# Optimization experiments

Measured on AMD Instinct MI355X. Metric: run time of the kernel, lower is better.

## Reference

```python
import jax, jax.numpy as jnp
import numpy as np

N, M, D = 1024, 1024, 512


def setup_inputs() -> dict:
    key = jax.random.key(0)
    ks = jax.random.split(key, 12)
    s = 1.0 / np.sqrt(D)
    return {
        "q": jax.random.normal(ks[0], (N, D), jnp.float32),
        "k": jax.random.normal(ks[1], (M, D), jnp.float32),
        "v": jax.random.normal(ks[2], (M, D), jnp.float32),
        "mask": jax.random.randint(ks[3], (N, M), 0, 2) > 0,
        "Wq": jax.random.normal(ks[4], (D, D), jnp.float32) * s,
        "bq": jax.random.normal(ks[5], (D,), jnp.float32) * s,
        "Wk": jax.random.normal(ks[6], (D, D), jnp.float32) * s,
        "bk": jax.random.normal(ks[7], (D,), jnp.float32) * s,
        "Wv": jax.random.normal(ks[8], (D, D), jnp.float32) * s,
        "bv": jax.random.normal(ks[9], (D,), jnp.float32) * s,
        "Ww": jax.random.normal(ks[10], (D,), jnp.float32) * s,
        "bw": jax.random.normal(ks[11], (1,), jnp.float32) * s,
    }


def reference(q, k, v, mask, Wq, bq, Wk, bk, Wv, bv, Ww, bw):
    # Linear projections (torch Linear: x @ W.T + b)
    qp = q @ Wq.T + bq  # [N, D]
    kp = k @ Wk.T + bk  # [M, D]
    vp = v @ Wv.T + bv  # [M, D]
    # Bahdanau additive score: W(tanh(q_n + k_m)) -> [N, M]
    h = jnp.tanh(qp[:, None, :] + kp[None, :, :])  # [N, M, D]
    scores = jnp.einsum('nmd,d->nm', h, Ww) + bw[0]
    scores = jnp.where(mask, scores, jnp.float32(-1000000.0))
    attn = jax.nn.softmax(scores, axis=1)  # softmax over M (dim 1)
    context = jnp.einsum('nm,md->nd', attn, vp)  # [N, D]
    return context
```

## Files before the change

kernel.cpp:

```cpp
#include <hip/hip_runtime.h>
#include <hip/hip_bf16.h>
#include <float.h>


#define NROWS 1024
#define DDIM  512
#define MDIM  1024

typedef __attribute__((ext_vector_type(8))) short s8v;
typedef __attribute__((ext_vector_type(4))) float f4v;
typedef __attribute__((ext_vector_type(2))) float v2f;

__device__ __forceinline__ ushort f2bf(float f) {
    unsigned u = __float_as_uint(f);
    u = u + 0x7FFFu + ((u >> 16) & 1u);
    return (ushort)(u >> 16);
}
__device__ __forceinline__ float bf2f(ushort h) {
    return __uint_as_float(((unsigned)h) << 16);
}

__device__ __forceinline__ void load_lds16(const float* g, float* l) {
    __builtin_amdgcn_global_load_lds(
        (const __attribute__((address_space(1))) void*)g,
        (__attribute__((address_space(3))) void*)l, 16, 0, 0);
}

__global__ __launch_bounds__(256) void proj_gemm(
    const float* __restrict__ q, const float* __restrict__ kk_,
    const float* __restrict__ v,
    const float* __restrict__ Wq, const float* __restrict__ bq,
    const float* __restrict__ Wk, const float* __restrict__ bk,
    const float* __restrict__ Wv, const float* __restrict__ bv,
    float* __restrict__ eq, float* __restrict__ ekT,
    ushort* __restrict__ vph, ushort* __restrict__ vpl,
    float* __restrict__ S, float CS)
{
    __shared__ ushort Ah[4096], Al[4096], Bh[4096], Bl[4096];

    const float* A; const float* B; const float* bias;
    int biasRow;
    if (blockIdx.z == 0)      { A = q;   B = Wq;  bias = bq; biasRow = 0; }
    else if (blockIdx.z == 1) { A = Wk;  B = kk_; bias = bk; biasRow = 1; }
    else                      { A = Wv;  B = v;   bias = bv; biasRow = 1; }

    const int bi = (blockIdx.z == 0) ? blockIdx.x : blockIdx.y;
    const int bj = (blockIdx.z == 0) ? blockIdx.y : blockIdx.x;

    const int t    = threadIdx.x;
    const int lane = t & 63;
    const int w    = t >> 6;
    const int lm   = lane & 15;
    const int lq   = lane >> 4;
    const int i0   = bi * 64;
    const int j0   = bj * 64;
    const int mh   = (w >> 1) * 32;
    const int nh   = (w & 1) * 32;

    if (blockIdx.z == 0) {
        const int jb = blockIdx.x * 8 + blockIdx.y;
        float4 zz = {0.f, 0.f, 0.f, 0.f};
#pragma unroll
        for (int p = 0; p < 8; ++p)
            *(float4*)&S[(size_t)jb * 8192 + (t + p * 256) * 4] = zz;
    }

    f4v acc[2][2] = {{{0.f,0.f,0.f,0.f},{0.f,0.f,0.f,0.f}},
                     {{0.f,0.f,0.f,0.f},{0.f,0.f,0.f,0.f}}};
    float4 pa[4], pb[4];

    const int sr = t >> 4, sc4 = t & 15;
#pragma unroll
    for (int p = 0; p < 4; ++p) {
        int r = sr + p * 16;
        pa[p] = *(const float4*)&A[(size_t)(i0 + r) * DDIM + sc4 * 4];
        pb[p] = *(const float4*)&B[(size_t)(j0 + r) * DDIM + sc4 * 4];
    }

    for (int kc = 0; kc < 8; ++kc) {
        __syncthreads();
#pragma unroll
        for (int p = 0; p < 4; ++p) {
            int r = sr + p * 16;
            int ad = r * 64 + (((sc4 >> 1) ^ (r & 7)) << 3) + (sc4 & 1) * 4;
            float af[4] = {pa[p].x, pa[p].y, pa[p].z, pa[p].w};
            float bf[4] = {pb[p].x, pb[p].y, pb[p].z, pb[p].w};
            ushort ah4[4], al4[4], bh4[4], bl4[4];
#pragma unroll
            for (int e = 0; e < 4; ++e) {
                ah4[e] = f2bf(af[e]); al4[e] = f2bf(af[e] - bf2f(ah4[e]));
                bh4[e] = f2bf(bf[e]); bl4[e] = f2bf(bf[e] - bf2f(bh4[e]));
            }
            *(ushort4*)&Ah[ad] = *(ushort4*)ah4;
            *(ushort4*)&Al[ad] = *(ushort4*)al4;
            *(ushort4*)&Bh[ad] = *(ushort4*)bh4;
            *(ushort4*)&Bl[ad] = *(ushort4*)bl4;
        }
        __syncthreads();
        if (kc < 7) {
            const int k0 = (kc + 1) * 64;
#pragma unroll
            for (int p = 0; p < 4; ++p) {
                int r = sr + p * 16;
                pa[p] = *(const float4*)&A[(size_t)(i0 + r) * DDIM + k0 + sc4 * 4];
                pb[p] = *(const float4*)&B[(size_t)(j0 + r) * DDIM + k0 + sc4 * 4];
            }
        }
#pragma unroll
        for (int ks = 0; ks < 2; ++ks) {
            const int kb = ks * 4 + lq;
            s8v afh[2], afl[2], bfh[2], bfl[2];
#pragma unroll
            for (int g = 0; g < 2; ++g) {
                int ra = mh + g * 16 + lm;
                int rb = nh + g * 16 + lm;
                int aa = ra * 64 + ((kb ^ (ra & 7)) << 3);
                int ab = rb * 64 + ((kb ^ (rb & 7)) << 3);
                afh[g] = *(const s8v*)&Ah[aa];
                afl[g] = *(const s8v*)&Al[aa];
                bfh[g] = *(const s8v*)&Bh[ab];
                bfl[g] = *(const s8v*)&Bl[ab];
            }
#pragma unroll
            for (int mi = 0; mi < 2; ++mi)
#pragma unroll
                for (int ni = 0; ni < 2; ++ni) {
                    acc[mi][ni] = __builtin_amdgcn_mfma_f32_16x16x32_bf16(
                        afh[mi], bfh[ni], acc[mi][ni], 0, 0, 0);
                    acc[mi][ni] = __builtin_amdgcn_mfma_f32_16x16x32_bf16(
                        afh[mi], bfl[ni], acc[mi][ni], 0, 0, 0);
                    acc[mi][ni] = __builtin_amdgcn_mfma_f32_16x16x32_bf16(
                        afl[mi], bfh[ni], acc[mi][ni], 0, 0, 0);
                }
        }
    }

    const float CLAMP = 8192.0f;
#pragma unroll
    for (int mi = 0; mi < 2; ++mi) {
#pragma unroll
        for (int ni = 0; ni < 2; ++ni) {
#pragma unroll
            for (int p = 0; p < 4; ++p) {
                int row = i0 + mh + mi * 16 + lq * 4 + p;
                int col = j0 + nh + ni * 16 + lm;
                float val = acc[mi][ni][p] + (biasRow ? bias[row] : bias[col]);
                if (blockIdx.z == 0) {
                    eq[(size_t)row * 512 + col] =
                        fminf(__builtin_amdgcn_exp2f(val * CS), CLAMP);
                } else if (blockIdx.z == 1) {
                    ekT[(size_t)row * 1024 + col] =
                        fminf(__builtin_amdgcn_exp2f(val * CS), CLAMP);
                } else {
                    ushort h = f2bf(val);
                    vph[(size_t)row * 1024 + col] = h;
                    vpl[(size_t)row * 1024 + col] = f2bf(val - bf2f(h));
                }
            }
        }
    }
}

#define DCH  32
#define SMCH 128
__global__ __launch_bounds__(256) void score_kernel(const float* __restrict__ eq,
                                                    const float* __restrict__ ekT,
                                                    const float* __restrict__ Ww,
                                                    float* __restrict__ S)
{
    __shared__ __align__(16) float ks[DCH * SMCH];
    __shared__ __align__(16) float es[16 * DCH];
    __shared__ __align__(16) float wws[DCH];
    const int t    = threadIdx.x;
    const int lane = t & 63;
    const int w    = t >> 6;
    const int m0   = blockIdx.x * SMCH;
    const int n0   = blockIdx.y * 16;
    const int dbase = blockIdx.z * 256;

    v2f acc[4] = {};
    const v2f one2 = {1.f, 1.f};

    for (int dc = 0; dc < 256; dc += DCH) {
        const int d0 = dbase + dc;
        __syncthreads();
#pragma unroll
        for (int i = 0; i < 4; ++i) {
            int r2 = w * 8 + i * 2;
            const float* g = ekT + (size_t)(d0 + r2 + (lane >> 5)) * MDIM
                             + m0 + (lane & 31) * 4;
            load_lds16(g, &ks[r2 * SMCH]);
        }
#pragma unroll
        for (int p = 0; p < 2; ++p) {
            int idx = t + p * 256;
            int nl = idx >> 5, dd = idx & 31;
            es[nl * DCH + dd] = eq[(size_t)(n0 + nl) * DDIM + d0 + dd];
        }
        if (t < DCH) wws[t] = Ww[d0 + t];
        __syncthreads();

#pragma unroll
        for (int dq = 0; dq < DCH; dq += 4) {
            v2f k0 = *(const v2f*)&ks[(dq + 0) * SMCH + lane * 2];
            v2f k1 = *(const v2f*)&ks[(dq + 1) * SMCH + lane * 2];
            v2f k2 = *(const v2f*)&ks[(dq + 2) * SMCH + lane * 2];
            v2f k3 = *(const v2f*)&ks[(dq + 3) * SMCH + lane * 2];
            float4 wg = *(const float4*)&wws[dq];
#pragma unroll
            for (int nn = 0; nn < 4; ++nn) {
                float4 eg = *(const float4*)&es[(w * 4 + nn) * DCH + dq];
                v2f A0 = __builtin_elementwise_fma(k0, (v2f){eg.x, eg.x}, one2);
                v2f A1 = __builtin_elementwise_fma(k1, (v2f){eg.y, eg.y}, one2);
                v2f A2 = __builtin_elementwise_fma(k2, (v2f){eg.z, eg.z}, one2);
                v2f A3 = __builtin_elementwise_fma(k3, (v2f){eg.w, eg.w}, one2);
                v2f n01 = __builtin_elementwise_fma((v2f){wg.y, wg.y}, A0,
                                                    (v2f){wg.x, wg.x} * A1);
                v2f d01 = A0 * A1;
                v2f n23 = __builtin_elementwise_fma((v2f){wg.w, wg.w}, A2,
                                                    (v2f){wg.z, wg.z} * A3);
                v2f d23 = A2 * A3;
                v2f num = __builtin_elementwise_fma(n01, d23, n23 * d01);
                v2f den = d01 * d23;
                v2f r = {__builtin_amdgcn_rcpf(den.x), __builtin_amdgcn_rcpf(den.y)};
                acc[nn] = __builtin_elementwise_fma(num, r, acc[nn]);
            }
        }
    }

    const float C2 = -2.8853900817779268f;
    const int m = m0 + lane * 2;
#pragma unroll
    for (int nn = 0; nn < 4; ++nn) {
        int n = n0 + w * 4 + nn;
        atomicAdd(&S[(size_t)n * MDIM + m],     acc[nn].x * C2);
        atomicAdd(&S[(size_t)n * MDIM + m + 1], acc[nn].y * C2);
    }
}

__global__ __launch_bounds__(256) void combine_kernel(const float* __restrict__ S,
                                                      const int* __restrict__ mask,
                                                      ushort* __restrict__ Ph,
                                                      ushort* __restrict__ Pl,
                                                      float* __restrict__ rsum)
{
    __shared__ float red[4];
    const int n = blockIdx.x, t = threadIdx.x;
    const int lane = t & 63, w = t >> 6;

    float4 s  = *(const float4*)&S[(size_t)n * MDIM + t * 4];
    int4   mk = *(const int4*)&mask[(size_t)n * MDIM + t * 4];
    float p0 = mk.x ? __builtin_amdgcn_exp2f(s.x) : 0.f;
    float p1 = mk.y ? __builtin_amdgcn_exp2f(s.y) : 0.f;
    float p2 = mk.z ? __builtin_amdgcn_exp2f(s.z) : 0.f;
    float p3 = mk.w ? __builtin_amdgcn_exp2f(s.w) : 0.f;

    ushort h[4] = {f2bf(p0), f2bf(p1), f2bf(p2), f2bf(p3)};
    ushort l[4] = {f2bf(p0 - bf2f(h[0])), f2bf(p1 - bf2f(h[1])),
                   f2bf(p2 - bf2f(h[2])), f2bf(p3 - bf2f(h[3]))};
    *(ushort4*)&Ph[(size_t)n * MDIM + t * 4] = *(ushort4*)h;
    *(ushort4*)&Pl[(size_t)n * MDIM + t * 4] = *(ushort4*)l;

    float rs = (p0 + p1) + (p2 + p3);
#pragma unroll
    for (int off = 32; off; off >>= 1) rs += __shfl_xor(rs, off);
    if (lane == 0) red[w] = rs;
    __syncthreads();
    if (t == 0) rsum[n] = (red[0] + red[1]) + (red[2] + red[3]);
}

__global__ __launch_bounds__(256) void ctx_gemm(const ushort* __restrict__ Ph,
                                                const ushort* __restrict__ Pl,
                                                const ushort* __restrict__ vph,
                                                const ushort* __restrict__ vpl,
                                                const float* __restrict__ rsum,
                                                float* __restrict__ out)
{
    const int t    = threadIdx.x;
    const int lane = t & 63;
    const int w    = t >> 6;
    const int lm   = lane & 15;
    const int lq   = lane >> 4;
    const int d0   = blockIdx.x * 64 + w * 16;
    const int n0   = blockIdx.y * 16;

    const ushort* pAh = Ph  + (size_t)(n0 + lm) * MDIM + lq * 8;
    const ushort* pAl = Pl  + (size_t)(n0 + lm) * MDIM + lq * 8;
    const ushort* pBh = vph + (size_t)(d0 + lm) * MDIM + lq * 8;
    const ushort* pBl = vpl + (size_t)(d0 + lm) * MDIM + lq * 8;

    f4v acc = {0.f, 0.f, 0.f, 0.f};
#pragma unroll 4
    for (int m0 = 0; m0 < MDIM; m0 += 32) {
        s8v ah = *(const s8v*)(pAh + m0);
        s8v al = *(const s8v*)(pAl + m0);
        s8v bh = *(const s8v*)(pBh + m0);
        s8v bl = *(const s8v*)(pBl + m0);
        acc = __builtin_amdgcn_mfma_f32_16x16x32_bf16(ah, bh, acc, 0, 0, 0);
        acc = __builtin_amdgcn_mfma_f32_16x16x32_bf16(ah, bl, acc, 0, 0, 0);
        acc = __builtin_amdgcn_mfma_f32_16x16x32_bf16(al, bh, acc, 0, 0, 0);
    }

#pragma unroll
    for (int p = 0; p < 4; ++p) {
        int nrow = n0 + lq * 4 + p;
        float inv = __builtin_amdgcn_rcpf(rsum[nrow]);
        out[(size_t)nrow * DDIM + d0 + lm] = acc[p] * inv;
    }
}

extern "C" void kernel_launch(void* const* d_in, const int* in_sizes, int n_in,
                              void* d_out, int out_size, void* d_ws, size_t ws_size,
                              hipStream_t stream)
{
    const float* q    = (const float*)d_in[0];
    const float* k    = (const float*)d_in[1];
    const float* v    = (const float*)d_in[2];
    const int*   mask = (const int*)d_in[3];
    const float* Wq   = (const float*)d_in[4];
    const float* bq   = (const float*)d_in[5];
    const float* Wk   = (const float*)d_in[6];
    const float* bk   = (const float*)d_in[7];
    const float* Wv   = (const float*)d_in[8];
    const float* bv   = (const float*)d_in[9];
    const float* Ww   = (const float*)d_in[10];

    float* ws    = (float*)d_ws;
    float* eq    = ws;
    float* ekT   = ws + 524288;
    ushort* vph  = (ushort*)(ws + 1048576);
    ushort* vpl  = (ushort*)(ws + 1310720);
    float* S     = ws + 1572864;
    float* rsum  = ws + 2621440;
    ushort* Ph   = (ushort*)ws;
    ushort* Pl   = (ushort*)(ws + 524288);
    float* out   = (float*)d_out;

    const float CS = 2.8853900817779268f;

    proj_gemm<<<dim3(16, 8, 3), dim3(256), 0, stream>>>(q, k, v, Wq, bq, Wk, bk,
                                                        Wv, bv, eq, ekT,
                                                        vph, vpl, S, CS);
    score_kernel<<<dim3(8, 64, 2), dim3(256), 0, stream>>>(eq, ekT, Ww, S);
    combine_kernel<<<dim3(1024), dim3(256), 0, stream>>>(S, mask, Ph, Pl, rsum);
    ctx_gemm<<<dim3(8, 64), dim3(256), 0, stream>>>(Ph, Pl, vph, vpl, rsum, out);
}
```

Before: 181.4 us.

## Fuse softmax combine into context GEMM and preload score operands once

Removes the separate combine kernel. ctx_gemm now reads the raw scores and mask directly, computes the masked exp2, splits it into hi/lo bf16 and accumulates row sums via shuffles before feeding the MFMAs. This saves one launch and the Ph/Pl/rsum round trip through memory. The cost is that the exp and bf16 split are recomputed in every one of the 8 d-column blocks, and fp32 scores plus int mask are read in place of bf16 pairs. Separately, score_kernel now loads the full 256-wide eq slice and Ww into LDS once per block instead of once per d-chunk, which uses more LDS.

```diff
diff --git a/kernel.cpp b/kernel.cpp
--- a/kernel.cpp
+++ b/kernel.cpp
@@ -169,8 +169,8 @@
                                                     float* __restrict__ S)
 {
     __shared__ __align__(16) float ks[DCH * SMCH];
-    __shared__ __align__(16) float es[16 * DCH];
-    __shared__ __align__(16) float wws[DCH];
+    __shared__ __align__(16) float es[16 * 256];
+    __shared__ __align__(16) float wws[256];
     const int t    = threadIdx.x;
     const int lane = t & 63;
     const int w    = t >> 6;
@@ -178,6 +178,15 @@
     const int n0   = blockIdx.y * 16;
     const int dbase = blockIdx.z * 256;
 
+#pragma unroll
+    for (int p = 0; p < 4; ++p) {
+        int idx = t + p * 256;
+        int nl = idx >> 6, dd4 = idx & 63;
+        *(float4*)&es[nl * 256 + dd4 * 4] =
+            *(const float4*)&eq[(size_t)(n0 + nl) * DDIM + dbase + dd4 * 4];
+    }
+    wws[t] = Ww[dbase + t];
+
     v2f acc[4] = {};
     const v2f one2 = {1.f, 1.f};
 
@@ -191,13 +200,6 @@
                              + m0 + (lane & 31) * 4;
             load_lds16(g, &ks[r2 * SMCH]);
         }
-#pragma unroll
-        for (int p = 0; p < 2; ++p) {
-            int idx = t + p * 256;
-            int nl = idx >> 5, dd = idx & 31;
-            es[nl * DCH + dd] = eq[(size_t)(n0 + nl) * DDIM + d0 + dd];
-        }
-        if (t < DCH) wws[t] = Ww[d0 + t];
         __syncthreads();
 
 #pragma unroll
@@ -206,10 +208,10 @@
             v2f k1 = *(const v2f*)&ks[(dq + 1) * SMCH + lane * 2];
             v2f k2 = *(const v2f*)&ks[(dq + 2) * SMCH + lane * 2];
             v2f k3 = *(const v2f*)&ks[(dq + 3) * SMCH + lane * 2];
-            float4 wg = *(const float4*)&wws[dq];
+            float4 wg = *(const float4*)&wws[dc + dq];
 #pragma unroll
             for (int nn = 0; nn < 4; ++nn) {
-                float4 eg = *(const float4*)&es[(w * 4 + nn) * DCH + dq];
+                float4 eg = *(const float4*)&es[(w * 4 + nn) * 256 + dc + dq];
                 v2f A0 = __builtin_elementwise_fma(k0, (v2f){eg.x, eg.x}, one2);
                 v2f A1 = __builtin_elementwise_fma(k1, (v2f){eg.y, eg.y}, one2);
                 v2f A2 = __builtin_elementwise_fma(k2, (v2f){eg.z, eg.z}, one2);
@@ -238,42 +240,10 @@
     }
 }
 
-__global__ __launch_bounds__(256) void combine_kernel(const float* __restrict__ S,
-                                                      const int* __restrict__ mask,
-                                                      ushort* __restrict__ Ph,
-                                                      ushort* __restrict__ Pl,
-                                                      float* __restrict__ rsum)
-{
-    __shared__ float red[4];
-    const int n = blockIdx.x, t = threadIdx.x;
-    const int lane = t & 63, w = t >> 6;
-
-    float4 s  = *(const float4*)&S[(size_t)n * MDIM + t * 4];
-    int4   mk = *(const int4*)&mask[(size_t)n * MDIM + t * 4];
-    float p0 = mk.x ? __builtin_amdgcn_exp2f(s.x) : 0.f;
-    float p1 = mk.y ? __builtin_amdgcn_exp2f(s.y) : 0.f;
-    float p2 = mk.z ? __builtin_amdgcn_exp2f(s.z) : 0.f;
-    float p3 = mk.w ? __builtin_amdgcn_exp2f(s.w) : 0.f;
-
-    ushort h[4] = {f2bf(p0), f2bf(p1), f2bf(p2), f2bf(p3)};
-    ushort l[4] = {f2bf(p0 - bf2f(h[0])), f2bf(p1 - bf2f(h[1])),
-                   f2bf(p2 - bf2f(h[2])), f2bf(p3 - bf2f(h[3]))};
-    *(ushort4*)&Ph[(size_t)n * MDIM + t * 4] = *(ushort4*)h;
-    *(ushort4*)&Pl[(size_t)n * MDIM + t * 4] = *(ushort4*)l;
-
-    float rs = (p0 + p1) + (p2 + p3);
-#pragma unroll
-    for (int off = 32; off; off >>= 1) rs += __shfl_xor(rs, off);
-    if (lane == 0) red[w] = rs;
-    __syncthreads();
-    if (t == 0) rsum[n] = (red[0] + red[1]) + (red[2] + red[3]);
-}
-
-__global__ __launch_bounds__(256) void ctx_gemm(const ushort* __restrict__ Ph,
-                                                const ushort* __restrict__ Pl,
+__global__ __launch_bounds__(256) void ctx_gemm(const float* __restrict__ S,
+                                                const int* __restrict__ mask,
                                                 const ushort* __restrict__ vph,
                                                 const ushort* __restrict__ vpl,
-                                                const float* __restrict__ rsum,
                                                 float* __restrict__ out)
 {
     const int t    = threadIdx.x;
@@ -284,16 +254,37 @@
     const int d0   = blockIdx.x * 64 + w * 16;
     const int n0   = blockIdx.y * 16;
 
-    const ushort* pAh = Ph  + (size_t)(n0 + lm) * MDIM + lq * 8;
-    const ushort* pAl = Pl  + (size_t)(n0 + lm) * MDIM + lq * 8;
+    const float*  pS = S    + (size_t)(n0 + lm) * MDIM + lq * 8;
+    const int*    pM = mask + (size_t)(n0 + lm) * MDIM + lq * 8;
     const ushort* pBh = vph + (size_t)(d0 + lm) * MDIM + lq * 8;
     const ushort* pBl = vpl + (size_t)(d0 + lm) * MDIM + lq * 8;
 
     f4v acc = {0.f, 0.f, 0.f, 0.f};
+    float rs = 0.f;
 #pragma unroll 4
     for (int m0 = 0; m0 < MDIM; m0 += 32) {
-        s8v ah = *(const s8v*)(pAh + m0);
-        s8v al = *(const s8v*)(pAl + m0);
+        float4 sA = *(const float4*)(pS + m0);
+        float4 sB = *(const float4*)(pS + m0 + 4);
+        int4   mA = *(const int4*)(pM + m0);
+        int4   mB = *(const int4*)(pM + m0 + 4);
+        float pv[8];
+        pv[0] = mA.x ? __builtin_amdgcn_exp2f(sA.x) : 0.f;
+        pv[1] = mA.y ? __builtin_amdgcn_exp2f(sA.y) : 0.f;
+        pv[2] = mA.z ? __builtin_amdgcn_exp2f(sA.z) : 0.f;
+        pv[3] = mA.w ? __builtin_amdgcn_exp2f(sA.w) : 0.f;
+        pv[4] = mB.x ? __builtin_amdgcn_exp2f(sB.x) : 0.f;
+        pv[5] = mB.y ? __builtin_amdgcn_exp2f(sB.y) : 0.f;
+        pv[6] = mB.z ? __builtin_amdgcn_exp2f(sB.z) : 0.f;
+        pv[7] = mB.w ? __builtin_amdgcn_exp2f(sB.w) : 0.f;
+        ushort hh[8], ll[8];
+#pragma unroll
+        for (int j = 0; j < 8; ++j) {
+            hh[j] = f2bf(pv[j]);
+            ll[j] = f2bf(pv[j] - bf2f(hh[j]));
+            rs += pv[j];
+        }
+        s8v ah = *(const s8v*)hh;
+        s8v al = *(const s8v*)ll;
         s8v bh = *(const s8v*)(pBh + m0);
         s8v bl = *(const s8v*)(pBl + m0);
         acc = __builtin_amdgcn_mfma_f32_16x16x32_bf16(ah, bh, acc, 0, 0, 0);
@@ -301,10 +292,14 @@
         acc = __builtin_amdgcn_mfma_f32_16x16x32_bf16(al, bh, acc, 0, 0, 0);
     }
 
+    rs += __shfl_xor(rs, 16);
+    rs += __shfl_xor(rs, 32);
+
 #pragma unroll
     for (int p = 0; p < 4; ++p) {
         int nrow = n0 + lq * 4 + p;
-        float inv = __builtin_amdgcn_rcpf(rsum[nrow]);
+        float rtot = __shfl(rs, lq * 4 + p);
+        float inv = __builtin_amdgcn_rcpf(rtot);
         out[(size_t)nrow * DDIM + d0 + lm] = acc[p] * inv;
     }
 }
@@ -331,9 +326,6 @@
     ushort* vph  = (ushort*)(ws + 1048576);
     ushort* vpl  = (ushort*)(ws + 1310720);
     float* S     = ws + 1572864;
-    float* rsum  = ws + 2621440;
-    ushort* Ph   = (ushort*)ws;
-    ushort* Pl   = (ushort*)(ws + 524288);
     float* out   = (float*)d_out;
 
     const float CS = 2.8853900817779268f;
@@ -342,6 +334,5 @@
                                                         Wv, bv, eq, ekT,
                                                         vph, vpl, S, CS);
     score_kernel<<<dim3(8, 64, 2), dim3(256), 0, stream>>>(eq, ekT, Ww, S);
-    combine_kernel<<<dim3(1024), dim3(256), 0, stream>>>(S, mask, Ph, Pl, rsum);
-    ctx_gemm<<<dim3(8, 64), dim3(256), 0, stream>>>(Ph, Pl, vph, vpl, rsum, out);
-}
+    ctx_gemm<<<dim3(8, 64), dim3(256), 0, stream>>>(S, mask, vph, vpl, out);
+}
```

Result: slower. 191.6 us (+5.6%).

## Halve proj tile width, split ctx GEMM over M with atomics, preload eq tile

Applied to the files above, without the earlier changes.

The projection GEMM tile changes from 64x64 to 64x32 and the grid doubles, giving more blocks for the three projections. The proj kernel also zeroes the output buffer so the context GEMM can be split in two along M and accumulate with atomicAdd, doubling its block count. The score kernel now loads its whole 16x256 eq slice and Ww slice into LDS once instead of per 32-wide chunk, removing per-iteration global loads. The cost is more LDS in the score kernel, atomic traffic on the output, and smaller per-block reuse in the projection GEMM.

```diff
diff --git a/kernel.cpp b/kernel.cpp
--- a/kernel.cpp
+++ b/kernel.cpp
@@ -34,9 +34,10 @@
     const float* __restrict__ Wv, const float* __restrict__ bv,
     float* __restrict__ eq, float* __restrict__ ekT,
     ushort* __restrict__ vph, ushort* __restrict__ vpl,
-    float* __restrict__ S, float CS)
-{
-    __shared__ ushort Ah[4096], Al[4096], Bh[4096], Bl[4096];
+    float* __restrict__ S, float* __restrict__ outz, float CS)
+{
+    __shared__ ushort Ah[4096], Al[4096];
+    __shared__ ushort Bh[2048], Bl[2048];
 
     const float* A; const float* B; const float* bias;
     int biasRow;
@@ -44,38 +45,42 @@
     else if (blockIdx.z == 1) { A = Wk;  B = kk_; bias = bk; biasRow = 1; }
     else                      { A = Wv;  B = v;   bias = bv; biasRow = 1; }
 
-    const int bi = (blockIdx.z == 0) ? blockIdx.x : blockIdx.y;
-    const int bj = (blockIdx.z == 0) ? blockIdx.y : blockIdx.x;
-
     const int t    = threadIdx.x;
+    const int flat = blockIdx.y * 16 + blockIdx.x;
+    const int bi = (blockIdx.z == 0) ? (flat >> 4) : (flat >> 5);
+    const int bj = (blockIdx.z == 0) ? (flat & 15) : (flat & 31);
+
     const int lane = t & 63;
     const int w    = t >> 6;
     const int lm   = lane & 15;
     const int lq   = lane >> 4;
     const int i0   = bi * 64;
-    const int j0   = bj * 64;
+    const int j0   = bj * 32;
     const int mh   = (w >> 1) * 32;
-    const int nh   = (w & 1) * 32;
+    const int nh   = (w & 1) * 16;
 
     if (blockIdx.z == 0) {
-        const int jb = blockIdx.x * 8 + blockIdx.y;
         float4 zz = {0.f, 0.f, 0.f, 0.f};
 #pragma unroll
-        for (int p = 0; p < 8; ++p)
-            *(float4*)&S[(size_t)jb * 8192 + (t + p * 256) * 4] = zz;
-    }
-
-    f4v acc[2][2] = {{{0.f,0.f,0.f,0.f},{0.f,0.f,0.f,0.f}},
-                     {{0.f,0.f,0.f,0.f},{0.f,0.f,0.f,0.f}}};
-    float4 pa[4], pb[4];
+        for (int p = 0; p < 4; ++p)
+            *(float4*)&S[(size_t)flat * 4096 + (t + p * 256) * 4] = zz;
+    } else if (blockIdx.z == 2) {
+        float4 zz = {0.f, 0.f, 0.f, 0.f};
+#pragma unroll
+        for (int p = 0; p < 2; ++p)
+            *(float4*)&outz[(size_t)flat * 2048 + (t + p * 256) * 4] = zz;
+    }
+
+    f4v acc[2] = {{0.f,0.f,0.f,0.f},{0.f,0.f,0.f,0.f}};
+    float4 pa[4], pb[2];
 
     const int sr = t >> 4, sc4 = t & 15;
 #pragma unroll
-    for (int p = 0; p < 4; ++p) {
-        int r = sr + p * 16;
-        pa[p] = *(const float4*)&A[(size_t)(i0 + r) * DDIM + sc4 * 4];
-        pb[p] = *(const float4*)&B[(size_t)(j0 + r) * DDIM + sc4 * 4];
-    }
+    for (int p = 0; p < 4; ++p)
+        pa[p] = *(const float4*)&A[(size_t)(i0 + sr + p * 16) * DDIM + sc4 * 4];
+#pragma unroll
+    for (int p = 0; p < 2; ++p)
+        pb[p] = *(const float4*)&B[(size_t)(j0 + sr + p * 16) * DDIM + sc4 * 4];
 
     for (int kc = 0; kc < 8; ++kc) {
         __syncthreads();
@@ -84,81 +89,84 @@
             int r = sr + p * 16;
             int ad = r * 64 + (((sc4 >> 1) ^ (r & 7)) << 3) + (sc4 & 1) * 4;
             float af[4] = {pa[p].x, pa[p].y, pa[p].z, pa[p].w};
+            ushort h4[4], l4[4];
+#pragma unroll
+            for (int e = 0; e < 4; ++e) {
+                h4[e] = f2bf(af[e]); l4[e] = f2bf(af[e] - bf2f(h4[e]));
+            }
+            *(ushort4*)&Ah[ad] = *(ushort4*)h4;
+            *(ushort4*)&Al[ad] = *(ushort4*)l4;
+        }
+#pragma unroll
+        for (int p = 0; p < 2; ++p) {
+            int r = sr + p * 16;
+            int ad = r * 64 + (((sc4 >> 1) ^ (r & 7)) << 3) + (sc4 & 1) * 4;
             float bf[4] = {pb[p].x, pb[p].y, pb[p].z, pb[p].w};
-            ushort ah4[4], al4[4], bh4[4], bl4[4];
+            ushort h4[4], l4[4];
 #pragma unroll
             for (int e = 0; e < 4; ++e) {
-                ah4[e] = f2bf(af[e]); al4[e] = f2bf(af[e] - bf2f(ah4[e]));
-                bh4[e] = f2bf(bf[e]); bl4[e] = f2bf(bf[e] - bf2f(bh4[e]));
-            }
-            *(ushort4*)&Ah[ad] = *(ushort4*)ah4;
-            *(ushort4*)&Al[ad] = *(ushort4*)al4;
-            *(ushort4*)&Bh[ad] = *(ushort4*)bh4;
-            *(ushort4*)&Bl[ad] = *(ushort4*)bl4;
+                h4[e] = f2bf(bf[e]); l4[e] = f2bf(bf[e] - bf2f(h4[e]));
+            }
+            *(ushort4*)&Bh[ad] = *(ushort4*)h4;
+            *(ushort4*)&Bl[ad] = *(ushort4*)l4;
         }
         __syncthreads();
         if (kc < 7) {
             const int k0 = (kc + 1) * 64;
 #pragma unroll
-            for (int p = 0; p < 4; ++p) {
-                int r = sr + p * 16;
-                pa[p] = *(const float4*)&A[(size_t)(i0 + r) * DDIM + k0 + sc4 * 4];
-                pb[p] = *(const float4*)&B[(size_t)(j0 + r) * DDIM + k0 + sc4 * 4];
-            }
+            for (int p = 0; p < 4; ++p)
+                pa[p] = *(const float4*)&A[(size_t)(i0 + sr + p * 16) * DDIM + k0 + sc4 * 4];
+#pragma unroll
+            for (int p = 0; p < 2; ++p)
+                pb[p] = *(const float4*)&B[(size_t)(j0 + sr + p * 16) * DDIM + k0 + sc4 * 4];
         }
 #pragma unroll
         for (int ks = 0; ks < 2; ++ks) {
             const int kb = ks * 4 + lq;
-            s8v afh[2], afl[2], bfh[2], bfl[2];
-#pragma unroll
-            for (int g = 0; g < 2; ++g) {
-                int ra = mh + g * 16 + lm;
-                int rb = nh + g * 16 + lm;
+            s8v afh[2], afl[2];
+#pragma unroll
+            for (int mi = 0; mi < 2; ++mi) {
+                int ra = mh + mi * 16 + lm;
                 int aa = ra * 64 + ((kb ^ (ra & 7)) << 3);
-                int ab = rb * 64 + ((kb ^ (rb & 7)) << 3);
-                afh[g] = *(const s8v*)&Ah[aa];
-                afl[g] = *(const s8v*)&Al[aa];
-                bfh[g] = *(const s8v*)&Bh[ab];
-                bfl[g] = *(const s8v*)&Bl[ab];
-            }
-#pragma unroll
-            for (int mi = 0; mi < 2; ++mi)
-#pragma unroll
-                for (int ni = 0; ni < 2; ++ni) {
-                    acc[mi][ni] = __builtin_amdgcn_mfma_f32_16x16x32_bf16(
-                        afh[mi], bfh[ni], acc[mi][ni], 0, 0, 0);
-                    acc[mi][ni] = __builtin_amdgcn_mfma_f32_16x16x32_bf16(
-                        afh[mi], bfl[ni], acc[mi][ni], 0, 0, 0);
-                    acc[mi][ni] = __builtin_amdgcn_mfma_f32_16x16x32_bf16(
-                        afl[mi], bfh[ni], acc[mi][ni], 0, 0, 0);
-                }
+                afh[mi] = *(const s8v*)&Ah[aa];
+                afl[mi] = *(const s8v*)&Al[aa];
+            }
+            int rb = nh + lm;
+            int ab = rb * 64 + ((kb ^ (rb & 7)) << 3);
+            s8v bfh = *(const s8v*)&Bh[ab];
+            s8v bfl = *(const s8v*)&Bl[ab];
+#pragma unroll
+            for (int mi = 0; mi < 2; ++mi) {
+                acc[mi] = __builtin_amdgcn_mfma_f32_16x16x32_bf16(afh[mi], bfh, acc[mi], 0, 0, 0);
+                acc[mi] = __builtin_amdgcn_mfma_f32_16x16x32_bf16(afh[mi], bfl, acc[mi], 0, 0, 0);
+                acc[mi] = __builtin_amdgcn_mfma_f32_16x16x32_bf16(afl[mi], bfh, acc[mi], 0, 0, 0);
+            }
         }
     }
 
     const float CLAMP = 8192.0f;
+    const int C = (blockIdx.z == 0) ? 512 : 1024;
 #pragma unroll
     for (int mi = 0; mi < 2; ++mi) {
 #pragma unroll
-        for (int ni = 0; ni < 2; ++ni) {
-#pragma unroll
-            for (int p = 0; p < 4; ++p) {
-                int row = i0 + mh + mi * 16 + lq * 4 + p;
-                int col = j0 + nh + ni * 16 + lm;
-                float val = acc[mi][ni][p] + (biasRow ? bias[row] : bias[col]);
-                if (blockIdx.z == 0) {
-                    eq[(size_t)row * 512 + col] =
-                        fminf(__builtin_amdgcn_exp2f(val * CS), CLAMP);
-                } else if (blockIdx.z == 1) {
-                    ekT[(size_t)row * 1024 + col] =
-                        fminf(__builtin_amdgcn_exp2f(val * CS), CLAMP);
-                } else {
-                    ushort h = f2bf(val);
-                    vph[(size_t)row * 1024 + col] = h;
-                    vpl[(size_t)row * 1024 + col] = f2bf(val - bf2f(h));
-                }
-            }
-        }
-    }
+        for (int p = 0; p < 4; ++p) {
+            int row = i0 + mh + mi * 16 + lq * 4 + p;
+            int col = j0 + nh + lm;
+            float val = acc[mi][p] + (biasRow ? bias[row] : bias[col]);
+            if (blockIdx.z == 0) {
+                eq[(size_t)row * 512 + col] =
+                    fminf(__builtin_amdgcn_exp2f(val * CS), CLAMP);
+            } else if (blockIdx.z == 1) {
+                ekT[(size_t)row * 1024 + col] =
+                    fminf(__builtin_amdgcn_exp2f(val * CS), CLAMP);
+            } else {
+                ushort h = f2bf(val);
+                vph[(size_t)row * 1024 + col] = h;
+                vpl[(size_t)row * 1024 + col] = f2bf(val - bf2f(h));
+            }
+        }
+    }
+    (void)C;
 }
 
 #define DCH  32
@@ -169,8 +177,8 @@
                                                     float* __restrict__ S)
 {
     __shared__ __align__(16) float ks[DCH * SMCH];
-    __shared__ __align__(16) float es[16 * DCH];
-    __shared__ __align__(16) float wws[DCH];
+    __shared__ __align__(16) float es[16 * 256];
+    __shared__ __align__(16) float wws[256];
     const int t    = threadIdx.x;
     const int lane = t & 63;
     const int w    = t >> 6;
@@ -178,6 +186,15 @@
     const int n0   = blockIdx.y * 16;
     const int dbase = blockIdx.z * 256;
 
+#pragma unroll
+    for (int p = 0; p < 4; ++p) {
+        int idx = t + p * 256;
+        int nl = idx >> 6, dd4 = idx & 63;
+        *(float4*)&es[nl * 256 + dd4 * 4] =
+            *(const float4*)&eq[(size_t)(n0 + nl) * DDIM + dbase + dd4 * 4];
+    }
+    wws[t] = Ww[dbase + t];
+
     v2f acc[4] = {};
     const v2f one2 = {1.f, 1.f};
 
@@ -191,13 +208,6 @@
                              + m0 + (lane & 31) * 4;
             load_lds16(g, &ks[r2 * SMCH]);
         }
-#pragma unroll
-        for (int p = 0; p < 2; ++p) {
-            int idx = t + p * 256;
-            int nl = idx >> 5, dd = idx & 31;
-            es[nl * DCH + dd] = eq[(size_t)(n0 + nl) * DDIM + d0 + dd];
-        }
-        if (t < DCH) wws[t] = Ww[d0 + t];
         __syncthreads();
 
 #pragma unroll
@@ -206,10 +216,10 @@
             v2f k1 = *(const v2f*)&ks[(dq + 1) * SMCH + lane * 2];
             v2f k2 = *(const v2f*)&ks[(dq + 2) * SMCH + lane * 2];
             v2f k3 = *(const v2f*)&ks[(dq + 3) * SMCH + lane * 2];
-            float4 wg = *(const float4*)&wws[dq];
+            float4 wg = *(const float4*)&wws[dc + dq];
 #pragma unroll
             for (int nn = 0; nn < 4; ++nn) {
-                float4 eg = *(const float4*)&es[(w * 4 + nn) * DCH + dq];
+                float4 eg = *(const float4*)&es[(w * 4 + nn) * 256 + dc + dq];
                 v2f A0 = __builtin_elementwise_fma(k0, (v2f){eg.x, eg.x}, one2);
                 v2f A1 = __builtin_elementwise_fma(k1, (v2f){eg.y, eg.y}, one2);
                 v2f A2 = __builtin_elementwise_fma(k2, (v2f){eg.z, eg.z}, one2);
@@ -283,15 +293,16 @@
     const int lq   = lane >> 4;
     const int d0   = blockIdx.x * 64 + w * 16;
     const int n0   = blockIdx.y * 16;
-
-    const ushort* pAh = Ph  + (size_t)(n0 + lm) * MDIM + lq * 8;
-    const ushort* pAl = Pl  + (size_t)(n0 + lm) * MDIM + lq * 8;
-    const ushort* pBh = vph + (size_t)(d0 + lm) * MDIM + lq * 8;
-    const ushort* pBl = vpl + (size_t)(d0 + lm) * MDIM + lq * 8;
+    const int mb   = blockIdx.z * 512;
+
+    const ushort* pAh = Ph  + (size_t)(n0 + lm) * MDIM + mb + lq * 8;
+    const ushort* pAl = Pl  + (size_t)(n0 + lm) * MDIM + mb + lq * 8;
+    const ushort* pBh = vph + (size_t)(d0 + lm) * MDIM + mb + lq * 8;
+    const ushort* pBl = vpl + (size_t)(d0 + lm) * MDIM + mb + lq * 8;
 
     f4v acc = {0.f, 0.f, 0.f, 0.f};
 #pragma unroll 4
-    for (int m0 = 0; m0 < MDIM; m0 += 32) {
+    for (int m0 = 0; m0 < 512; m0 += 32) {
         s8v ah = *(const s8v*)(pAh + m0);
         s8v al = *(const s8v*)(pAl + m0);
         s8v bh = *(const s8v*)(pBh + m0);
@@ -305,7 +316,7 @@
     for (int p = 0; p < 4; ++p) {
         int nrow = n0 + lq * 4 + p;
         float inv = __builtin_amdgcn_rcpf(rsum[nrow]);
-        out[(size_t)nrow * DDIM + d0 + lm] = acc[p] * inv;
+        atomicAdd(&out[(size_t)nrow * DDIM + d0 + lm], acc[p] * inv);
     }
 }
 
@@ -338,10 +349,10 @@
 
     const float CS = 2.8853900817779268f;
 
-    proj_gemm<<<dim3(16, 8, 3), dim3(256), 0, stream>>>(q, k, v, Wq, bq, Wk, bk,
-                                                        Wv, bv, eq, ekT,
-                                                        vph, vpl, S, CS);
+    proj_gemm<<<dim3(16, 16, 3), dim3(256), 0, stream>>>(q, k, v, Wq, bq, Wk, bk,
+                                                         Wv, bv, eq, ekT,
+                                                         vph, vpl, S, out, CS);
     score_kernel<<<dim3(8, 64, 2), dim3(256), 0, stream>>>(eq, ekT, Ww, S);
     combine_kernel<<<dim3(1024), dim3(256), 0, stream>>>(S, mask, Ph, Pl, rsum);
-    ctx_gemm<<<dim3(8, 64), dim3(256), 0, stream>>>(Ph, Pl, vph, vpl, rsum, out);
-}
+    ctx_gemm<<<dim3(8, 64, 2), dim3(256), 0, stream>>>(Ph, Pl, vph, vpl, rsum, out);
+}
```

Result: no change. 181.4 us (-0.0%).
